# Optimization experiments

Hardware: AMD Instinct MI355X
Metric: run time of the kernel (lower is better)

The kernel has to match this reference:

```python
import jax, jax.numpy as jnp
import numpy as np

D_MODEL = 1024
N_HEADS = 16
D_HEAD = D_MODEL // N_HEADS
D_FF = 4096
BATCH = 2
SEQ = 2048
LN_EPS = 1e-5


def setup_inputs() -> dict:
    key = jax.random.key(0)
    ks = jax.random.split(key, 12)
    s = 1.0 / np.sqrt(D_MODEL)
    x = jax.random.normal(ks[0], (BATCH, SEQ, D_MODEL), dtype=jnp.float32)
    mask = jnp.broadcast_to(jnp.tril(jnp.ones((SEQ, SEQ), jnp.int32)), (BATCH, SEQ, SEQ))
    return {
        "x": x,
        "mask": mask,
        # per-head projections stacked: [H, D, Dh] (bias=False in source)
        "Wq": jax.random.normal(ks[1], (N_HEADS, D_MODEL, D_HEAD), jnp.float32) * s,
        "Wk": jax.random.normal(ks[2], (N_HEADS, D_MODEL, D_HEAD), jnp.float32) * s,
        "Wv": jax.random.normal(ks[3], (N_HEADS, D_MODEL, D_HEAD), jnp.float32) * s,
        "Wo": jax.random.normal(ks[4], (D_MODEL, D_MODEL), jnp.float32) * s,
        "ln1_w": jnp.ones((D_MODEL,), jnp.float32),
        "ln1_b": jnp.zeros((D_MODEL,), jnp.float32),
        "ln2_w": jnp.ones((D_MODEL,), jnp.float32),
        "ln2_b": jnp.zeros((D_MODEL,), jnp.float32),
        "W1": jax.random.normal(ks[5], (D_MODEL, D_FF), jnp.float32) * s,
        "b1": jnp.zeros((D_FF,), jnp.float32),
        "W2": jax.random.normal(ks[6], (D_FF, D_MODEL), jnp.float32) * (1.0 / np.sqrt(D_FF)),
        "b2": jnp.zeros((D_MODEL,), jnp.float32),
    }


def layer_norm(x, w, b):
    mu = jnp.mean(x, axis=-1, keepdims=True)
    var = jnp.var(x, axis=-1, keepdims=True)
    return (x - mu) * jax.lax.rsqrt(var + LN_EPS) * w + b


def reference(x, mask, Wq, Wk, Wv, Wo, ln1_w, ln1_b, ln2_w, ln2_b, W1, b1, W2, b2):
    # pre-LN masked self-attention
    h = layer_norm(x, ln1_w, ln1_b)
    q = jnp.einsum("bsd,hde->bhse", h, Wq)  # [B,H,S,Dh]
    k = jnp.einsum("bsd,hde->bhse", h, Wk)
    v = jnp.einsum("bsd,hde->bhse", h, Wv)
    scores = jnp.einsum("bhse,bhte->bhst", q, k) / np.sqrt(D_HEAD)
    scores = jnp.where(mask[:, None, :, :].astype(bool), scores, -jnp.inf)
    weights = jax.nn.softmax(scores, axis=-1)
    attn = jnp.einsum("bhst,bhte->bhse", weights, v)  # [B,H,S,Dh]
    # concat heads (head order = last-dim order in torch.cat)
    concat = attn.transpose(0, 2, 1, 3).reshape(x.shape[0], x.shape[1], D_MODEL)
    att_out = concat @ Wo
    att_x = x + att_out
    # FFN with exact (erf) GELU, matching nn.GELU default
    h2 = layer_norm(att_x, ln2_w, ln2_b)
    ff = jax.nn.gelu(h2 @ W1 + b1, approximate=False) @ W2 + b2
    return att_x + ff
```

## Files before the change

### kernel.cpp

```cpp
#include <hip/hip_runtime.h>
#include <hip/hip_bf16.h>
#include <math.h>

#define D_MODEL 1024
#define N_HEADS 16
#define D_HEAD  64
#define D_FF    4096
#define BATCH   2
#define SEQ     2048
#define NTOK    (BATCH*SEQ)

typedef __hip_bfloat16 bf16;
typedef __attribute__((ext_vector_type(8))) short short8;
typedef __attribute__((ext_vector_type(4))) float floatx4;

template<typename TIN>
__global__ void ln_kernel(const TIN* __restrict__ x,
                          const float* __restrict__ w,
                          const float* __restrict__ b,
                          bf16* __restrict__ out) {
    int row = blockIdx.x;
    int tid = threadIdx.x;
    const long base = (long)row * D_MODEL;
    float v[4];
    float s = 0.f, sq = 0.f;
#pragma unroll
    for (int i = 0; i < 4; ++i) {
        float xv = (float)x[base + tid + i*256];
        v[i] = xv; s += xv; sq += xv*xv;
    }
    __shared__ float r1[256], r2[256];
    r1[tid] = s; r2[tid] = sq; __syncthreads();
    for (int off = 128; off > 0; off >>= 1) {
        if (tid < off) { r1[tid] += r1[tid+off]; r2[tid] += r2[tid+off]; }
        __syncthreads();
    }
    float mean = r1[0] * (1.f/D_MODEL);
    float var  = r2[0] * (1.f/D_MODEL) - mean*mean;
    float rstd = rsqrtf(var + 1e-5f);
#pragma unroll
    for (int i = 0; i < 4; ++i) {
        int c = tid + i*256;
        out[base + c] = __float2bfloat16((v[i] - mean) * rstd * w[c] + b[c]);
    }
}

__global__ __launch_bounds__(256) void wcvt_kernel(const float* __restrict__ W,
                                                   bf16* __restrict__ Wt,
                                                   int K, int N) {
    __shared__ float t[32][33];
    int n0 = blockIdx.x * 32, k0 = blockIdx.y * 32;
    int lx = threadIdx.x & 31, ly = threadIdx.x >> 5;
#pragma unroll
    for (int i = 0; i < 4; ++i) {
        int k = ly + i * 8;
        t[k][lx] = W[(long)(k0 + k) * N + n0 + lx];
    }
    __syncthreads();
#pragma unroll
    for (int i = 0; i < 4; ++i) {
        int n = ly + i * 8;
        Wt[(long)(n0 + n) * K + k0 + lx] = __float2bfloat16(t[lx][n]);
    }
}

__global__ __launch_bounds__(256) void wcvt_qkv(const float* __restrict__ Wq,
                                                const float* __restrict__ Wk,
                                                const float* __restrict__ Wv,
                                                bf16* __restrict__ outp) {
    __shared__ float t[32][33];
    int z = blockIdx.z, mat = z >> 4, head = z & 15;
    const float* W = (mat == 0 ? Wq : mat == 1 ? Wk : Wv) + (long)head * D_MODEL * D_HEAD;
    bf16* Wt = outp + (long)z * D_HEAD * D_MODEL;
    int n0 = blockIdx.x * 32, k0 = blockIdx.y * 32;
    int lx = threadIdx.x & 31, ly = threadIdx.x >> 5;
#pragma unroll
    for (int i = 0; i < 4; ++i) {
        int k = ly + i * 8;
        t[k][lx] = W[(long)(k0 + k) * D_HEAD + n0 + lx];
    }
    __syncthreads();
#pragma unroll
    for (int i = 0; i < 4; ++i) {
        int n = ly + i * 8;
        Wt[(long)(n0 + n) * D_MODEL + k0 + lx] = __float2bfloat16(t[lx][n]);
    }
}

template<int ROWS>
__device__ inline void stage_tile(const bf16* g, int gstride, short* lds) {
    int lane = threadIdx.x & 63, wave = threadIdx.x >> 6;
#pragma unroll
    for (int it = 0; it < ROWS / 64; ++it) {
        int c = wave + it * 4;
        const bf16* gp = g + (long)(c * 16 + (lane >> 2)) * gstride + (lane & 3) * 8;
        short* lp = lds + c * 512 + lane * 8;
        __builtin_amdgcn_global_load_lds(
            (const __attribute__((address_space(1))) void*)gp,
            (__attribute__((address_space(3))) void*)lp, 16, 0, 0);
    }
}

template<int BM, int BN, int BIAS, int ACT, int RES, int OUTBF16>
__device__ inline void gemm_bf_body(const bf16* __restrict__ A, int lda,
                                    const bf16* __restrict__ Wt, int K,
                                    const float* __restrict__ bias,
                                    const float* __restrict__ resid,
                                    void* __restrict__ Cout, int ldc,
                                    int row0, int col0, short* As, short* Bs) {
    constexpr int MI = BM / 32;
    constexpr int NR = BN / 32;
    int tid  = threadIdx.x;
    int wave = tid >> 6, lane = tid & 63;
    int quad = lane >> 4, l16 = lane & 15;
    int wm = (wave >> 1) * (BM / 2);
    int wn = (wave & 1) * (BN / 2);

    floatx4 acc[MI][NR];
#pragma unroll
    for (int mi = 0; mi < MI; ++mi)
#pragma unroll
        for (int ni = 0; ni < NR; ++ni)
            acc[mi][ni] = (floatx4){0.f, 0.f, 0.f, 0.f};

    for (int k0 = 0; k0 < K; k0 += 64) {
        stage_tile<BM>(A  + (long)row0 * lda + k0,      lda, As);
        stage_tile<BM>(A  + (long)row0 * lda + k0 + 32, lda, As + BM * 32);
        stage_tile<BN>(Wt + (long)col0 * K   + k0,      K,   Bs);
        stage_tile<BN>(Wt + (long)col0 * K   + k0 + 32, K,   Bs + BN * 32);
        __syncthreads();

#pragma unroll
        for (int p = 0; p < 2; ++p) {
            const short* Ap = As + p * BM * 32;
            const short* Bp = Bs + p * BN * 32;
            short8 af[MI], bfr[NR];
#pragma unroll
            for (int mi = 0; mi < MI; ++mi)
                af[mi] = *(const short8*)&Ap[(wm + mi * 16 + l16) * 32 + quad * 8];
#pragma unroll
            for (int ni = 0; ni < NR; ++ni)
                bfr[ni] = *(const short8*)&Bp[(wn + ni * 16 + l16) * 32 + quad * 8];
#pragma unroll
            for (int mi = 0; mi < MI; ++mi)
#pragma unroll
                for (int ni = 0; ni < NR; ++ni)
                    acc[mi][ni] = __builtin_amdgcn_mfma_f32_16x16x32_bf16(
                        af[mi], bfr[ni], acc[mi][ni], 0, 0, 0);
        }
        __syncthreads();
    }

#pragma unroll
    for (int mi = 0; mi < MI; ++mi) {
#pragma unroll
        for (int ni = 0; ni < NR; ++ni) {
#pragma unroll
            for (int r = 0; r < 4; ++r) {
                int row = row0 + wm + mi * 16 + quad * 4 + r;
                int col = col0 + wn + ni * 16 + l16;
                float v = acc[mi][ni][r];
                if (BIAS) v += bias[col];
                if (ACT == 1) v = 0.5f * v * (1.f + erff(v * 0.70710678118654752f));
                long idx = (long)row * ldc + col;
                if (RES == 1) v += resid[idx];
                if (OUTBF16) ((bf16*)Cout)[idx] = __float2bfloat16(v);
                else         ((float*)Cout)[idx] = v;
            }
        }
    }
}

template<int BM, int BN, int BIAS, int ACT, int RES, int OUTBF16>
__global__ __launch_bounds__(256) void mfma_gemm_bf(
    const bf16* __restrict__ A, int lda,
    const bf16* __restrict__ Wt, int K,
    const float* __restrict__ bias, const float* __restrict__ resid,
    void* __restrict__ Cout, int ldc)
{
    __shared__ short As[BM * 64];
    __shared__ short Bs[BN * 64];
    gemm_bf_body<BM, BN, BIAS, ACT, RES, OUTBF16>(
        A, lda, Wt, K, bias, resid, Cout, ldc,
        blockIdx.y * BM, blockIdx.x * BN, As, Bs);
}

struct QkvOut { bf16* o[3]; };
__global__ __launch_bounds__(256) void qkv_kernel(const bf16* __restrict__ h1,
                                                  const bf16* __restrict__ wqkv,
                                                  QkvOut a) {
    int z = blockIdx.z;
    int bh = z / 3, mat = z - bh * 3;
    int b = bh >> 4, head = bh & 15;
    const bf16* Ab = h1 + (long)b * SEQ * D_MODEL;
    const bf16* Wt = wqkv + (long)(mat * 16 + head) * D_HEAD * D_MODEL;
    bf16* Cb = a.o[mat] + (long)bh * SEQ * D_HEAD;
    __shared__ short As[128 * 64];
    __shared__ short Bs[64 * 64];
    gemm_bf_body<128, 64, 0, 0, 0, 1>(
        Ab, D_MODEL, Wt, D_MODEL, nullptr, nullptr, Cb, D_HEAD,
        blockIdx.y * 128, 0, As, Bs);
}

__global__ __launch_bounds__(256) void fattn_mfma(const bf16* __restrict__ q,
                                                  const bf16* __restrict__ k,
                                                  const bf16* __restrict__ v,
                                                  bf16* __restrict__ concat) {
    int tile = (blockIdx.x + blockIdx.y) & 31;
    int bh = blockIdx.y;
    int b  = bh >> 4, h = bh & 15;
    int tid = threadIdx.x;
    int wave = tid >> 6, lane = tid & 63;
    int quad = lane >> 4, l16 = lane & 15;
    const long base = (long)bh * SEQ * D_HEAD;
    const int r0g = tile * 64;

    __shared__ short Ks[64 * 72];
    __shared__ short Vt[64 * 72];
    __shared__ short Ps[4][16 * 72];

    short8 qf0, qf1;
    {
        const short* qrow = (const short*)(q + base + (long)(r0g + wave * 16 + l16) * D_HEAD);
        qf0 = *(const short8*)(qrow + quad * 8);
        qf1 = *(const short8*)(qrow + 32 + quad * 8);
#pragma unroll
        for (int j = 0; j < 8; ++j) {
            float f0 = __uint_as_float(((unsigned)(unsigned short)qf0[j]) << 16) * 0.18033688f;
            float f1 = __uint_as_float(((unsigned)(unsigned short)qf1[j]) << 16) * 0.18033688f;
            qf0[j] = __builtin_bit_cast(short, __float2bfloat16(f0));
            qf1[j] = __builtin_bit_cast(short, __float2bfloat16(f1));
        }
    }

    short8 onesf;
    {
        short o1 = (l16 == 0) ? (short)0x3F80 : (short)0;
#pragma unroll
        for (int j = 0; j < 8; ++j) onesf[j] = o1;
    }

    floatx4 o[4];
#pragma unroll
    for (int nb = 0; nb < 4; ++nb) o[nb] = (floatx4){0.f, 0.f, 0.f, 0.f};
    floatx4 l4 = (floatx4){0.f, 0.f, 0.f, 0.f};

    for (int kt = 0; kt <= tile; ++kt) {
        __syncthreads();
        {
            int t = tid >> 2, c = tid & 3;
            const short* krow = (const short*)(k + base + (long)(kt * 64 + t) * D_HEAD);
            *(uint4*)&Ks[t * 72 + c * 16]     = *(const uint4*)(krow + c * 16);
            *(uint4*)&Ks[t * 72 + c * 16 + 8] = *(const uint4*)(krow + c * 16 + 8);
        }
        {
            int tp = (tid & 31) * 2;
            int d0 = ((tid >> 5) & 7) * 8;
            const short* v0 = (const short*)(v + base + (long)(kt * 64 + tp) * D_HEAD + d0);
            short va[8], vb[8];
            *(uint4*)va = *(const uint4*)v0;
            *(uint4*)vb = *(const uint4*)(v0 + D_HEAD);
#pragma unroll
            for (int j = 0; j < 8; ++j) {
                unsigned pk = (unsigned)(unsigned short)va[j] |
                              ((unsigned)(unsigned short)vb[j] << 16);
                *(unsigned*)&Vt[(d0 + j) * 72 + tp] = pk;
            }
        }
        __syncthreads();

        floatx4 s[4];
#pragma unroll
        for (int nb = 0; nb < 4; ++nb) {
            short8 kf0 = *(const short8*)&Ks[(nb * 16 + l16) * 72 + quad * 8];
            short8 kf1 = *(const short8*)&Ks[(nb * 16 + l16) * 72 + 32 + quad * 8];
            floatx4 z4 = (floatx4){0.f, 0.f, 0.f, 0.f};
            z4 = __builtin_amdgcn_mfma_f32_16x16x32_bf16(qf0, kf0, z4, 0, 0, 0);
            z4 = __builtin_amdgcn_mfma_f32_16x16x32_bf16(qf1, kf1, z4, 0, 0, 0);
            s[nb] = z4;
        }

        if (kt == tile) {
            const int qloc = wave * 16 + quad * 4;
#pragma unroll
            for (int nb = 0; nb < 4; ++nb)
#pragma unroll
                for (int r = 0; r < 4; ++r)
                    if ((nb * 16 + l16) > (qloc + r)) s[nb][r] = -1e30f;
        }

        short* Pw = &Ps[wave][0];
#pragma unroll
        for (int nb = 0; nb < 4; ++nb)
#pragma unroll
            for (int r = 0; r < 4; ++r) {
                float p = exp2f(s[nb][r]);
                Pw[(quad * 4 + r) * 72 + nb * 16 + l16] =
                    __builtin_bit_cast(short, __float2bfloat16(p));
            }

        short8 pf0 = *(const short8*)&Pw[l16 * 72 + quad * 8];
        short8 pf1 = *(const short8*)&Pw[l16 * 72 + 32 + quad * 8];
#pragma unroll
        for (int nb = 0; nb < 4; ++nb) {
            short8 vf0 = *(const short8*)&Vt[(nb * 16 + l16) * 72 + quad * 8];
            short8 vf1 = *(const short8*)&Vt[(nb * 16 + l16) * 72 + 32 + quad * 8];
            o[nb] = __builtin_amdgcn_mfma_f32_16x16x32_bf16(pf0, vf0, o[nb], 0, 0, 0);
            o[nb] = __builtin_amdgcn_mfma_f32_16x16x32_bf16(pf1, vf1, o[nb], 0, 0, 0);
        }
        l4 = __builtin_amdgcn_mfma_f32_16x16x32_bf16(pf0, onesf, l4, 0, 0, 0);
        l4 = __builtin_amdgcn_mfma_f32_16x16x32_bf16(pf1, onesf, l4, 0, 0, 0);
    }

    float linv[4];
#pragma unroll
    for (int r = 0; r < 4; ++r) {
        float lv = __shfl(l4[r], lane & 48);
        linv[r] = 1.f / lv;
    }
#pragma unroll
    for (int nb = 0; nb < 4; ++nb)
#pragma unroll
        for (int r = 0; r < 4; ++r) {
            int row = r0g + wave * 16 + quad * 4 + r;
            int col = h * D_HEAD + nb * 16 + l16;
            concat[(long)(b * SEQ + row) * D_MODEL + col] =
                __float2bfloat16(o[nb][r] * linv[r]);
        }
}

extern "C" void kernel_launch(void* const* d_in, const int* in_sizes, int n_in,
                              void* d_out, int out_size, void* d_ws, size_t ws_size,
                              hipStream_t stream) {
    const float* x    = (const float*)d_in[0];
    const float* Wq   = (const float*)d_in[2];
    const float* Wk   = (const float*)d_in[3];
    const float* Wv   = (const float*)d_in[4];
    const float* Wo   = (const float*)d_in[5];
    const float* ln1w = (const float*)d_in[6];
    const float* ln1b = (const float*)d_in[7];
    const float* ln2w = (const float*)d_in[8];
    const float* ln2b = (const float*)d_in[9];
    const float* W1   = (const float*)d_in[10];
    const float* b1   = (const float*)d_in[11];
    const float* W2   = (const float*)d_in[12];
    const float* b2   = (const float*)d_in[13];
    float* out = (float*)d_out;

    char* wsb = (char*)d_ws;
    const size_t MB = 1024*1024;
    bf16*  h1      = (bf16*)(wsb + 0*MB);
    bf16*  qb      = (bf16*)(wsb + 8*MB);
    bf16*  kb      = (bf16*)(wsb + 16*MB);
    bf16*  vb      = (bf16*)(wsb + 24*MB);
    bf16*  wqkv_bf = (bf16*)(wsb + 32*MB);
    bf16*  cc      = (bf16*)(wsb + 0*MB);
    bf16*  wo_bf   = (bf16*)(wsb + 8*MB);
    bf16*  w1_bf   = (bf16*)(wsb + 10*MB);
    bf16*  h2      = (bf16*)(wsb + 0*MB);
    bf16*  ff      = (bf16*)(wsb + 24*MB);
    bf16*  w2_bf   = (bf16*)(wsb + 8*MB);

    ln_kernel<float><<<NTOK, 256, 0, stream>>>(x, ln1w, ln1b, h1);

    wcvt_qkv<<<dim3(2, 32, 48), 256, 0, stream>>>(Wq, Wk, Wv, wqkv_bf);

    QkvOut qa; qa.o[0] = qb; qa.o[1] = kb; qa.o[2] = vb;
    qkv_kernel<<<dim3(1, 16, 96), 256, 0, stream>>>(h1, wqkv_bf, qa);

    fattn_mfma<<<dim3(SEQ/64, BATCH*N_HEADS), 256, 0, stream>>>(qb, kb, vb, cc);

    wcvt_kernel<<<dim3(D_MODEL/32, D_MODEL/32), 256, 0, stream>>>(Wo, wo_bf, D_MODEL, D_MODEL);
    wcvt_kernel<<<dim3(D_FF/32,    D_MODEL/32), 256, 0, stream>>>(W1, w1_bf, D_MODEL, D_FF);

    mfma_gemm_bf<64,128,0,0,1,0><<<dim3(8,64), 256, 0, stream>>>(
        cc, D_MODEL, wo_bf, D_MODEL, nullptr, x, out, D_MODEL);

    ln_kernel<float><<<NTOK, 256, 0, stream>>>(out, ln2w, ln2b, h2);

    mfma_gemm_bf<128,128,1,1,0,1><<<dim3(32,32), 256, 0, stream>>>(
        h2, D_MODEL, w1_bf, D_MODEL, b1, nullptr, ff, D_FF);

    wcvt_kernel<<<dim3(D_MODEL/32, D_FF/32), 256, 0, stream>>>(W2, w2_bf, D_FF, D_MODEL);

    mfma_gemm_bf<64,128,1,0,1,0><<<dim3(8,64), 256, 0, stream>>>(
        ff, D_FF, w2_bf, D_FF, b2, out, out, D_MODEL);
}
```

Baseline: 410.7 us.

## Process 128 query rows per attention block to reuse K/V tiles

```diff
diff --git a/kernel.cpp b/kernel.cpp
--- a/kernel.cpp
+++ b/kernel.cpp
@@ -206,31 +206,35 @@
                                                   const bf16* __restrict__ k,
                                                   const bf16* __restrict__ v,
                                                   bf16* __restrict__ concat) {
-    int tile = (blockIdx.x + blockIdx.y) & 31;
-    int bh = blockIdx.y;
+    int byr = blockIdx.y;
+    int tile = (byr < 8) ? byr : 23 - byr;
+    int bh = blockIdx.x;
     int b  = bh >> 4, h = bh & 15;
     int tid = threadIdx.x;
     int wave = tid >> 6, lane = tid & 63;
     int quad = lane >> 4, l16 = lane & 15;
     const long base = (long)bh * SEQ * D_HEAD;
-    const int r0g = tile * 64;
+    const int r0g = tile * 128;
 
     __shared__ short Ks[64 * 72];
     __shared__ short Vt[64 * 72];
-    __shared__ short Ps[4][16 * 72];
-
-    short8 qf0, qf1;
-    {
-        const short* qrow = (const short*)(q + base + (long)(r0g + wave * 16 + l16) * D_HEAD);
-        qf0 = *(const short8*)(qrow + quad * 8);
-        qf1 = *(const short8*)(qrow + 32 + quad * 8);
-#pragma unroll
-        for (int j = 0; j < 8; ++j) {
-            float f0 = __uint_as_float(((unsigned)(unsigned short)qf0[j]) << 16) * 0.18033688f;
-            float f1 = __uint_as_float(((unsigned)(unsigned short)qf1[j]) << 16) * 0.18033688f;
-            qf0[j] = __builtin_bit_cast(short, __float2bfloat16(f0));
-            qf1[j] = __builtin_bit_cast(short, __float2bfloat16(f1));
-        }
+    __shared__ short Ps[4][32 * 72];
+
+    short8 qf[2][2];
+#pragma unroll
+    for (int rb = 0; rb < 2; ++rb) {
+        const short* qrow = (const short*)(q + base +
+            (long)(r0g + wave * 32 + rb * 16 + l16) * D_HEAD);
+        qf[rb][0] = *(const short8*)(qrow + quad * 8);
+        qf[rb][1] = *(const short8*)(qrow + 32 + quad * 8);
+#pragma unroll
+        for (int c = 0; c < 2; ++c)
+#pragma unroll
+            for (int j = 0; j < 8; ++j) {
+                float f = __uint_as_float(((unsigned)(unsigned short)qf[rb][c][j]) << 16)
+                          * 0.18033688f;
+                qf[rb][c][j] = __builtin_bit_cast(short, __float2bfloat16(f));
+            }
     }
 
     short8 onesf;
@@ -240,12 +244,15 @@
         for (int j = 0; j < 8; ++j) onesf[j] = o1;
     }
 
-    floatx4 o[4];
-#pragma unroll
-    for (int nb = 0; nb < 4; ++nb) o[nb] = (floatx4){0.f, 0.f, 0.f, 0.f};
-    floatx4 l4 = (floatx4){0.f, 0.f, 0.f, 0.f};
-
-    for (int kt = 0; kt <= tile; ++kt) {
+    floatx4 o[2][4];
+#pragma unroll
+    for (int rb = 0; rb < 2; ++rb)
+#pragma unroll
+        for (int nb = 0; nb < 4; ++nb) o[rb][nb] = (floatx4){0.f, 0.f, 0.f, 0.f};
+    floatx4 l4[2] = {(floatx4){0.f,0.f,0.f,0.f}, (floatx4){0.f,0.f,0.f,0.f}};
+
+    const int ktmax = 2 * tile + 1;
+    for (int kt = 0; kt <= ktmax; ++kt) {
         __syncthreads();
         {
             int t = tid >> 2, c = tid & 3;
@@ -269,64 +276,89 @@
         }
         __syncthreads();
 
-        floatx4 s[4];
+        if (kt * 64 > r0g + wave * 32 + 31) continue;
+
+        floatx4 s[2][4];
 #pragma unroll
         for (int nb = 0; nb < 4; ++nb) {
             short8 kf0 = *(const short8*)&Ks[(nb * 16 + l16) * 72 + quad * 8];
             short8 kf1 = *(const short8*)&Ks[(nb * 16 + l16) * 72 + 32 + quad * 8];
-            floatx4 z4 = (floatx4){0.f, 0.f, 0.f, 0.f};
-            z4 = __builtin_amdgcn_mfma_f32_16x16x32_bf16(qf0, kf0, z4, 0, 0, 0);
-            z4 = __builtin_amdgcn_mfma_f32_16x16x32_bf16(qf1, kf1, z4, 0, 0, 0);
-            s[nb] = z4;
-        }
-
-        if (kt == tile) {
-            const int qloc = wave * 16 + quad * 4;
+#pragma unroll
+            for (int rb = 0; rb < 2; ++rb) {
+                floatx4 z4 = (floatx4){0.f, 0.f, 0.f, 0.f};
+                z4 = __builtin_amdgcn_mfma_f32_16x16x32_bf16(qf[rb][0], kf0, z4, 0, 0, 0);
+                z4 = __builtin_amdgcn_mfma_f32_16x16x32_bf16(qf[rb][1], kf1, z4, 0, 0, 0);
+                s[rb][nb] = z4;
+            }
+        }
+
+        if (kt >= 2 * tile) {
+#pragma unroll
+            for (int rb = 0; rb < 2; ++rb) {
+                int qg = r0g + wave * 32 + rb * 16 + quad * 4;
+#pragma unroll
+                for (int nb = 0; nb < 4; ++nb) {
+                    int kg = kt * 64 + nb * 16 + l16;
+#pragma unroll
+                    for (int r = 0; r < 4; ++r)
+                        if (kg > qg + r) s[rb][nb][r] = -1e30f;
+                }
+            }
+        }
+
+        short* Pw = &Ps[wave][0];
+#pragma unroll
+        for (int rb = 0; rb < 2; ++rb)
 #pragma unroll
             for (int nb = 0; nb < 4; ++nb)
 #pragma unroll
-                for (int r = 0; r < 4; ++r)
-                    if ((nb * 16 + l16) > (qloc + r)) s[nb][r] = -1e30f;
-        }
-
-        short* Pw = &Ps[wave][0];
-#pragma unroll
-        for (int nb = 0; nb < 4; ++nb)
-#pragma unroll
-            for (int r = 0; r < 4; ++r) {
-                float p = exp2f(s[nb][r]);
-                Pw[(quad * 4 + r) * 72 + nb * 16 + l16] =
-                    __builtin_bit_cast(short, __float2bfloat16(p));
-            }
-
-        short8 pf0 = *(const short8*)&Pw[l16 * 72 + quad * 8];
-        short8 pf1 = *(const short8*)&Pw[l16 * 72 + 32 + quad * 8];
+                for (int r = 0; r < 4; ++r) {
+                    float p = exp2f(s[rb][nb][r]);
+                    Pw[(rb * 16 + quad * 4 + r) * 72 + nb * 16 + l16] =
+                        __builtin_bit_cast(short, __float2bfloat16(p));
+                }
+
+        short8 pf[2][2];
+#pragma unroll
+        for (int rb = 0; rb < 2; ++rb) {
+            pf[rb][0] = *(const short8*)&Pw[(rb * 16 + l16) * 72 + quad * 8];
+            pf[rb][1] = *(const short8*)&Pw[(rb * 16 + l16) * 72 + 32 + quad * 8];
+        }
 #pragma unroll
         for (int nb = 0; nb < 4; ++nb) {
             short8 vf0 = *(const short8*)&Vt[(nb * 16 + l16) * 72 + quad * 8];
             short8 vf1 = *(const short8*)&Vt[(nb * 16 + l16) * 72 + 32 + quad * 8];
-            o[nb] = __builtin_amdgcn_mfma_f32_16x16x32_bf16(pf0, vf0, o[nb], 0, 0, 0);
-            o[nb] = __builtin_amdgcn_mfma_f32_16x16x32_bf16(pf1, vf1, o[nb], 0, 0, 0);
-        }
-        l4 = __builtin_amdgcn_mfma_f32_16x16x32_bf16(pf0, onesf, l4, 0, 0, 0);
-        l4 = __builtin_amdgcn_mfma_f32_16x16x32_bf16(pf1, onesf, l4, 0, 0, 0);
-    }
-
-    float linv[4];
-#pragma unroll
-    for (int r = 0; r < 4; ++r) {
-        float lv = __shfl(l4[r], lane & 48);
-        linv[r] = 1.f / lv;
-    }
-#pragma unroll
-    for (int nb = 0; nb < 4; ++nb)
+#pragma unroll
+            for (int rb = 0; rb < 2; ++rb) {
+                o[rb][nb] = __builtin_amdgcn_mfma_f32_16x16x32_bf16(pf[rb][0], vf0, o[rb][nb], 0, 0, 0);
+                o[rb][nb] = __builtin_amdgcn_mfma_f32_16x16x32_bf16(pf[rb][1], vf1, o[rb][nb], 0, 0, 0);
+            }
+        }
+#pragma unroll
+        for (int rb = 0; rb < 2; ++rb) {
+            l4[rb] = __builtin_amdgcn_mfma_f32_16x16x32_bf16(pf[rb][0], onesf, l4[rb], 0, 0, 0);
+            l4[rb] = __builtin_amdgcn_mfma_f32_16x16x32_bf16(pf[rb][1], onesf, l4[rb], 0, 0, 0);
+        }
+    }
+
+#pragma unroll
+    for (int rb = 0; rb < 2; ++rb) {
+        float linv[4];
 #pragma unroll
         for (int r = 0; r < 4; ++r) {
-            int row = r0g + wave * 16 + quad * 4 + r;
-            int col = h * D_HEAD + nb * 16 + l16;
-            concat[(long)(b * SEQ + row) * D_MODEL + col] =
-                __float2bfloat16(o[nb][r] * linv[r]);
-        }
+            float lv = __shfl(l4[rb][r], lane & 48);
+            linv[r] = 1.f / lv;
+        }
+#pragma unroll
+        for (int nb = 0; nb < 4; ++nb)
+#pragma unroll
+            for (int r = 0; r < 4; ++r) {
+                int row = r0g + wave * 32 + rb * 16 + quad * 4 + r;
+                int col = h * D_HEAD + nb * 16 + l16;
+                concat[(long)(b * SEQ + row) * D_MODEL + col] =
+                    __float2bfloat16(o[rb][nb][r] * linv[r]);
+            }
+    }
 }
 
 extern "C" void kernel_launch(void* const* d_in, const int* in_sizes, int n_in,
@@ -368,7 +400,7 @@
     QkvOut qa; qa.o[0] = qb; qa.o[1] = kb; qa.o[2] = vb;
     qkv_kernel<<<dim3(1, 16, 96), 256, 0, stream>>>(h1, wqkv_bf, qa);
 
-    fattn_mfma<<<dim3(SEQ/64, BATCH*N_HEADS), 256, 0, stream>>>(qb, kb, vb, cc);
+    fattn_mfma<<<dim3(BATCH*N_HEADS, SEQ/128), 256, 0, stream>>>(qb, kb, vb, cc);
 
     wcvt_kernel<<<dim3(D_MODEL/32, D_MODEL/32), 256, 0, stream>>>(Wo, wo_bf, D_MODEL, D_MODEL);
     wcvt_kernel<<<dim3(D_FF/32,    D_MODEL/32), 256, 0, stream>>>(W1, w1_bf, D_MODEL, D_FF);
```

Result: no change. 403.2 us (-1.8%).
